# Kernel optimization log

Measured on AMD Instinct MI355X. Metric: run time of the kernel, lower is better.

Reference implementation:

```python
import jax, jax.numpy as jnp
import numpy as np
import math

VOCAB = 390
D = 512
D_INNER = 2048
H = 8
DH = D // H
L = 6
MAX_SEQ = 1024
BATCH = 4
OUT = 2
PAD = 0
EPS = 1e-6


def sinusoid(max_seq, d):
    pos = np.arange(max_seq, dtype=np.float64)[:, None]
    i = np.arange(d, dtype=np.float64)[None, :]
    angle = (pos * np.exp(-np.log(10000.0) * i / d) * np.exp(np.log(10000.0) / d * (i % 2))
             + 0.5 * np.pi * (i % 2))
    return np.sin(angle)[None].astype(np.float32)  # [1, max_seq, d]


def setup_inputs() -> dict:
    key = jax.random.key(0)
    ks = jax.random.split(key, 16)
    s = 0.02
    emb = jax.random.uniform(ks[0], (VOCAB, D), jnp.float32, -0.1, 0.1)
    emb = emb.at[PAD].set(0.0)  # padding_idx row zeroed
    inp = {
        'x': jax.random.randint(ks[1], (BATCH, MAX_SEQ), 0, VOCAB, dtype=jnp.int64) if jax.config.jax_enable_x64 else jax.random.randint(ks[1], (BATCH, MAX_SEQ), 0, VOCAB, dtype=jnp.int32),
        'emb': emb,
        'pos': jnp.asarray(sinusoid(MAX_SEQ, D)),
        'Wq': jax.random.normal(ks[2], (L, D, D), jnp.float32) * s,
        'bq': jnp.zeros((L, D), jnp.float32),
        'Wk': jax.random.normal(ks[3], (L, D, D), jnp.float32) * s,
        'bk': jnp.zeros((L, D), jnp.float32),
        'Wv': jax.random.normal(ks[4], (L, D, D), jnp.float32) * s,
        'bv': jnp.zeros((L, D), jnp.float32),
        'Wo': jax.random.normal(ks[5], (L, D, D), jnp.float32) * s,
        'bo': jnp.zeros((L, D), jnp.float32),
        'E': jax.random.normal(ks[6], (L, MAX_SEQ, DH), jnp.float32),
        'W1': jax.random.normal(ks[7], (L, D, D_INNER), jnp.float32) * s,
        'b1': jnp.zeros((L, D_INNER), jnp.float32),
        'W2': jax.random.normal(ks[8], (L, D_INNER, D), jnp.float32) * s,
        'b2': jnp.zeros((L, D), jnp.float32),
        'ln1_s': jnp.ones((L, D), jnp.float32),
        'ln1_b': jnp.zeros((L, D), jnp.float32),
        'ln2_s': jnp.ones((L, D), jnp.float32),
        'ln2_b': jnp.zeros((L, D), jnp.float32),
        'Wf': jax.random.normal(ks[9], (D, OUT), jnp.float32) * s,
        'bf': jnp.zeros((OUT,), jnp.float32),
    }
    return inp


def _layernorm(x, scale, bias):
    mu = jnp.mean(x, axis=-1, keepdims=True)
    var = jnp.mean(jnp.square(x - mu), axis=-1, keepdims=True)
    return (x - mu) * jax.lax.rsqrt(var + EPS) * scale + bias


def _rel_attention(x, Wq, bq, Wk, bk, Wv, bv, Wo, bo, E):
    b, s, d = x.shape
    q = (x @ Wq + bq).reshape(b, s, H, DH).transpose(0, 2, 1, 3)  # [b,h,s,dh]
    k = (x @ Wk + bk).reshape(b, s, H, DH).transpose(0, 2, 1, 3)
    v = (x @ Wv + bv).reshape(b, s, H, DH).transpose(0, 2, 1, 3)
    m = MAX_SEQ  # len_q == len_k == max_seq -> full E
    QE = jnp.einsum('bhld,md->bhlm', q, E)  # [b,h,s,m]
    # qe masking: keep position j >= m-1-i for query row i
    keep = (jnp.arange(m)[None, :] >= (m - 1 - jnp.arange(s))[:, None]).astype(QE.dtype)
    QE = QE * keep
    # skewing trick: pad-left on last dim, reshape, drop first row
    padded = jnp.pad(QE, ((0, 0), (0, 0), (0, 0), (1, 0)))  # [b,h,s,m+1]
    Srel = padded.reshape(b, H, m + 1, s)[:, :, 1:, :]  # [b,h,m,s] == [b,h,s,s]
    logits = (jnp.einsum('bhqd,bhkd->bhqk', q, k) + Srel) / math.sqrt(DH)
    attn = jax.nn.softmax(logits, axis=-1)
    out = jnp.einsum('bhqk,bhkd->bhqd', attn, v)
    out = out.transpose(0, 2, 1, 3).reshape(b, s, d)
    return out @ Wo + bo


def reference(x, emb, pos, Wq, bq, Wk, bk, Wv, bv, Wo, bo, E, W1, b1, W2, b2,
              ln1_s, ln1_b, ln2_s, ln2_b, Wf, bf):
    h = emb[x] * math.sqrt(D)  # [b,s,d]
    h = h + pos[:, :h.shape[1], :]
    for i in range(L):
        attn = _rel_attention(h, Wq[i], bq[i], Wk[i], bk[i], Wv[i], bv[i], Wo[i], bo[i], E[i])
        h1 = _layernorm(attn + h, ln1_s[i], ln1_b[i])
        ffn = jax.nn.relu(h1 @ W1[i] + b1[i]) @ W2[i] + b2[i]
        h = _layernorm(h1 + ffn, ln2_s[i], ln2_b[i])
    return jnp.tanh(h[:, 0, :] @ Wf + bf)  # [b, OUT]
```

## Files before the change

kernel.cpp:

```cpp
#include <hip/hip_runtime.h>
#include <math.h>

#define BATCH  4
#define SEQ    1024
#define DM     512
#define DI     2048
#define NH     8
#define DH     64
#define NL     6
#define NOUT   2

typedef unsigned short u16;
typedef short s16x8 __attribute__((ext_vector_type(8)));
typedef float f32x4 __attribute__((ext_vector_type(4)));
typedef unsigned short u16x4 __attribute__((ext_vector_type(4)));

#define MFMA16(a, b, c) __builtin_amdgcn_mfma_f32_16x16x32_bf16((a), (b), (c), 0, 0, 0)

static constexpr float SQRT_D = 22.627416997969522f;

#define SLOT_WO   786432
#define SLOT_W1   1048576
#define SLOT_W2   2097152
#define SLOT_E    3145728
#define SLOT_SZ   3211264

__device__ __forceinline__ u16 f2b(float x) {
    union { float f; unsigned u; } v; v.f = x;
    unsigned r = v.u + 0x7fffu + ((v.u >> 16) & 1u);
    return (u16)(r >> 16);
}
__device__ __forceinline__ float b2f(u16 b) {
    union { unsigned u; float f; } v; v.u = ((unsigned)b) << 16; return v.f;
}

__global__ __launch_bounds__(256) void k_embed(const int* __restrict__ x,
                                               const float* __restrict__ emb,
                                               const float* __restrict__ pos,
                                               float* __restrict__ h,
                                               u16* __restrict__ hb) {
    const int idx = blockIdx.x * 256 + threadIdx.x;
    const int d4  = idx & 127;
    const int bs  = idx >> 7;
    const int s   = bs & (SEQ - 1);
    const int tok = x[bs];
    const float4 e = ((const float4*)emb)[tok * 128 + d4];
    const float4 p = ((const float4*)pos)[s * 128 + d4];
    float4 r;
    r.x = e.x * SQRT_D + p.x;  r.y = e.y * SQRT_D + p.y;
    r.z = e.z * SQRT_D + p.z;  r.w = e.w * SQRT_D + p.w;
    ((float4*)h)[idx] = r;
    u16x4 rb = { f2b(r.x), f2b(r.y), f2b(r.z), f2b(r.w) };
    ((u16x4*)hb)[idx] = rb;
}

__global__ __launch_bounds__(256) void k_conv(const float* __restrict__ Wq, const float* __restrict__ Wk,
                                              const float* __restrict__ Wv, const float* __restrict__ Wo,
                                              const float* __restrict__ W1, const float* __restrict__ W2,
                                              const float* __restrict__ E,
                                              u16* __restrict__ wbase, int layer0, int slot_stride) {
    const int ll = blockIdx.x / 3136;
    const int tb = blockIdx.x - ll * 3136;
    const int layer = layer0 + ll;
    u16* Wqkvt = wbase + (size_t)ll * slot_stride;
    u16* Wot   = Wqkvt + SLOT_WO;
    u16* W1t   = Wqkvt + SLOT_W1;
    u16* W2t   = Wqkvt + SLOT_W2;
    u16* Ebf   = Wqkvt + SLOT_E;

    if (tb >= 3072) {
        const int rem = tb - 3072;
        const int idx = rem * 1024 + threadIdx.x * 4;
        const float4 v = *(const float4*)(E + (size_t)layer * SEQ * DH + idx);
        u16x4 o = { f2b(v.x), f2b(v.y), f2b(v.z), f2b(v.w) };
        *(u16x4*)(Ebf + idx) = o;
        return;
    }
    __shared__ float T[32][33];
    const float* src; u16* dst; int Ksz, Nsz, tk, tn;
    if (tb < 768) {
        const int mat = tb >> 8, rem = tb & 255;
        src = (mat == 0 ? Wq : (mat == 1 ? Wk : Wv)) + (size_t)layer * DM * DM;
        dst = Wqkvt + (size_t)mat * DM * DM;
        Ksz = 512; Nsz = 512; tk = rem & 15; tn = rem >> 4;
    } else if (tb < 1024) {
        const int rem = tb - 768;
        src = Wo + (size_t)layer * DM * DM; dst = Wot;
        Ksz = 512; Nsz = 512; tk = rem & 15; tn = rem >> 4;
    } else if (tb < 2048) {
        const int rem = tb - 1024;
        src = W1 + (size_t)layer * DM * DI; dst = W1t;
        Ksz = 512; Nsz = 2048; tk = rem & 15; tn = rem >> 4;
    } else {
        const int rem = tb - 2048;
        src = W2 + (size_t)layer * DI * DM; dst = W2t;
        Ksz = 2048; Nsz = 512; tk = rem >> 4; tn = rem & 15;
    }
    {
        const int rr = threadIdx.x >> 3, c4 = (threadIdx.x & 7) << 2;
        const float4 v = *(const float4*)(src + (size_t)(tk * 32 + rr) * Nsz + tn * 32 + c4);
        T[rr][c4 + 0] = v.x; T[rr][c4 + 1] = v.y; T[rr][c4 + 2] = v.z; T[rr][c4 + 3] = v.w;
    }
    __syncthreads();
    {
        const int nl = threadIdx.x >> 3, k4 = (threadIdx.x & 7) << 2;
        u16x4 o = { f2b(T[k4 + 0][nl]), f2b(T[k4 + 1][nl]), f2b(T[k4 + 2][nl]), f2b(T[k4 + 3][nl]) };
        *(u16x4*)(dst + (size_t)(tn * 32 + nl) * Ksz + tk * 32 + k4) = o;
    }
}

__global__ __launch_bounds__(256) void k_vt(const u16* __restrict__ vb,
                                            u16* __restrict__ Vt) {
    __shared__ float T[32][33];
    const int tn = blockIdx.x;
    const int tk = blockIdx.y;
    const int b  = blockIdx.z;
    const u16* src = vb + (size_t)b * SEQ * DM;
    u16* dst = Vt + (size_t)b * DM * SEQ;
    {
        const int rr = threadIdx.x >> 3, c4 = (threadIdx.x & 7) << 2;
        const u16x4 v = *(const u16x4*)(src + (size_t)(tk * 32 + rr) * DM + tn * 32 + c4);
        T[rr][c4 + 0] = b2f(v.x); T[rr][c4 + 1] = b2f(v.y);
        T[rr][c4 + 2] = b2f(v.z); T[rr][c4 + 3] = b2f(v.w);
    }
    __syncthreads();
    {
        const int nl = threadIdx.x >> 3, k4 = (threadIdx.x & 7) << 2;
        u16x4 o = { f2b(T[k4 + 0][nl]), f2b(T[k4 + 1][nl]),
                    f2b(T[k4 + 2][nl]), f2b(T[k4 + 3][nl]) };
        *(u16x4*)(dst + (size_t)(tn * 32 + nl) * SEQ + tk * 32 + k4) = o;
    }
}

template <int RELU, int WRITE_BF16>
__global__ __launch_bounds__(256) void k_mm(const u16* __restrict__ A,
                                            const u16* __restrict__ Bt,
                                            const float* __restrict__ bias,
                                            float* __restrict__ Cf0,
                                            float* __restrict__ Cf1,
                                            u16* __restrict__ Cb,
                                            int K, int Kslice, int ldc) {
    __shared__ u16 As[128 * 40];
    __shared__ u16 Bs[128 * 40];

    const int n0 = blockIdx.x << 7;
    const int m0 = blockIdx.y << 7;
    const int zz = blockIdx.z;
    const int t  = threadIdx.x;
    const int lane = t & 63, w = t >> 6;
    const int n16 = lane & 15, quad = lane >> 4;
    const int wr = (w & 1) << 6;
    const int wc = (w >> 1) << 6;

    const f32x4 z = {0.f, 0.f, 0.f, 0.f};
    f32x4 acc[4][4];
#pragma unroll
    for (int i = 0; i < 4; ++i)
#pragma unroll
        for (int j = 0; j < 4; ++j) acc[i][j] = z;

    const int sr = t >> 2, sk = (t & 3) << 3;
    const int koff = zz * Kslice;
    const u16* Ag = A  + (size_t)(m0 + sr) * K + koff + sk;
    const u16* Bg = Bt + (size_t)(n0 + sr) * K + koff + sk;

    for (int k0 = 0; k0 < Kslice; k0 += 32) {
        __syncthreads();
        *(uint4*)&As[sr * 40 + sk]        = *(const uint4*)(Ag + k0);
        *(uint4*)&As[(sr + 64) * 40 + sk] = *(const uint4*)(Ag + (size_t)64 * K + k0);
        *(uint4*)&Bs[sr * 40 + sk]        = *(const uint4*)(Bg + k0);
        *(uint4*)&Bs[(sr + 64) * 40 + sk] = *(const uint4*)(Bg + (size_t)64 * K + k0);
        __syncthreads();

        s16x8 af[4], bfr[4];
#pragma unroll
        for (int rb = 0; rb < 4; ++rb)
            af[rb] = *(const s16x8*)&As[(wr + rb * 16 + n16) * 40 + quad * 8];
#pragma unroll
        for (int cb = 0; cb < 4; ++cb)
            bfr[cb] = *(const s16x8*)&Bs[(wc + cb * 16 + n16) * 40 + quad * 8];
#pragma unroll
        for (int rb = 0; rb < 4; ++rb)
#pragma unroll
            for (int cb = 0; cb < 4; ++cb)
                acc[rb][cb] = MFMA16(af[rb], bfr[cb], acc[rb][cb]);
    }

    float* Cf = zz ? Cf1 : Cf0;
#pragma unroll
    for (int cb = 0; cb < 4; ++cb) {
        const int col = n0 + wc + cb * 16 + n16;
        const float bv = (zz == 0) ? bias[col] : 0.f;
#pragma unroll
        for (int rb = 0; rb < 4; ++rb) {
#pragma unroll
            for (int rr = 0; rr < 4; ++rr) {
                const int row = m0 + wr + rb * 16 + quad * 4 + rr;
                float v = acc[rb][cb][rr] + bv;
                if (RELU) v = fmaxf(v, 0.f);
                const size_t idx = (size_t)row * ldc + col;
                if (WRITE_BF16) Cb[idx] = f2b(v);
                else            Cf[idx] = v;
            }
        }
    }
}

__global__ __launch_bounds__(256) void k_mm64(const u16* __restrict__ A,
                                              const u16* __restrict__ Bt,
                                              const float* __restrict__ bias0,
                                              const float* __restrict__ bias1,
                                              const float* __restrict__ bias2,
                                              u16* __restrict__ Cb,
                                              int K, int ldc, int seg_shift, size_t seg_stride) {
    __shared__ u16 As[64 * 72];
    __shared__ u16 Bs[128 * 72];

    const int n0 = blockIdx.x << 7;
    const int m0 = blockIdx.y << 6;
    const int t  = threadIdx.x;
    const int lane = t & 63, w = t >> 6;
    const int n16 = lane & 15, quad = lane >> 4;
    const int wc = w << 5;
    const int r = t >> 3, o = (t & 7) << 3;

    const f32x4 z = {0.f, 0.f, 0.f, 0.f};
    f32x4 acc[4][2];
#pragma unroll
    for (int i = 0; i < 4; ++i) { acc[i][0] = z; acc[i][1] = z; }

    const u16* Ag = A  + (size_t)(m0 + r) * K + o;
    const u16* Bg = Bt + (size_t)(n0 + r) * K + o;

    for (int k0 = 0; k0 < K; k0 += 64) {
        __syncthreads();
        *(uint4*)&As[r * 72 + o]        = *(const uint4*)(Ag + k0);
        *(uint4*)&As[(r + 32) * 72 + o] = *(const uint4*)(Ag + (size_t)32 * K + k0);
        *(uint4*)&Bs[r * 72 + o]        = *(const uint4*)(Bg + k0);
        *(uint4*)&Bs[(r + 32) * 72 + o] = *(const uint4*)(Bg + (size_t)32 * K + k0);
        *(uint4*)&Bs[(r + 64) * 72 + o] = *(const uint4*)(Bg + (size_t)64 * K + k0);
        *(uint4*)&Bs[(r + 96) * 72 + o] = *(const uint4*)(Bg + (size_t)96 * K + k0);
        __syncthreads();

#pragma unroll
        for (int ks = 0; ks < 2; ++ks) {
            s16x8 af[4], bfr[2];
#pragma unroll
            for (int rb = 0; rb < 4; ++rb)
                af[rb] = *(const s16x8*)&As[(rb * 16 + n16) * 72 + ks * 32 + quad * 8];
#pragma unroll
            for (int cb = 0; cb < 2; ++cb)
                bfr[cb] = *(const s16x8*)&Bs[(wc + cb * 16 + n16) * 72 + ks * 32 + quad * 8];
#pragma unroll
            for (int rb = 0; rb < 4; ++rb)
#pragma unroll
                for (int cb = 0; cb < 2; ++cb)
                    acc[rb][cb] = MFMA16(af[rb], bfr[cb], acc[rb][cb]);
        }
    }

    const int sel = n0 >> seg_shift;
    const int colbase = (n0 & ((1 << seg_shift) - 1)) + wc;
    const float* bias = (sel == 0) ? bias0 : (sel == 1 ? bias1 : bias2);
    const size_t cbase = (size_t)sel * seg_stride;
#pragma unroll
    for (int cb = 0; cb < 2; ++cb) {
        const int col = colbase + cb * 16 + n16;
        const float bv = bias[col];
#pragma unroll
        for (int rb = 0; rb < 4; ++rb)
#pragma unroll
            for (int rr = 0; rr < 4; ++rr) {
                const int row = m0 + rb * 16 + quad * 4 + rr;
                Cb[cbase + (size_t)row * ldc + col] = f2b(acc[rb][cb][rr] + bv);
            }
    }
}

__global__ __launch_bounds__(256) void k_attn(const u16* __restrict__ Qg,
                                              const u16* __restrict__ Kg,
                                              const u16* __restrict__ Vt,
                                              const u16* __restrict__ Eg,
                                              u16* __restrict__ Og) {
    __shared__ u16 Ks[64 * 72];
    __shared__ u16 Vts[64 * 72];
    __shared__ u16 Ps[64 * 72];
    __shared__ u16 Es[128 * 72];
    __shared__ u16 arena[128 * 72];

    const int i0 = blockIdx.x << 6;
    const int hd = blockIdx.y;
    const int b  = blockIdx.z;
    const int t  = threadIdx.x;
    const int lane = t & 63;
    const int n16 = lane & 15;
    const int quad = lane >> 4;
    const int rw = (t >> 6) << 4;
    const int ir_base = rw + (quad << 2);
    const int a_last = i0 >> 6;
    const int eb0 = 960 - i0;

    const size_t gb  = (size_t)b * SEQ * DM + hd * DH;
    const size_t vtb = ((size_t)b * DM + hd * DH) * SEQ;

    const int r = t >> 3;
    const int o = (t & 7) << 3;

    const u16* qp = Qg + gb + (size_t)(i0 + rw + n16) * DM + quad * 8;
    const s16x8 qa0 = *(const s16x8*)qp;
    const s16x8 qa1 = *(const s16x8*)(qp + 32);

    uint4 kr0 = *(const uint4*)(Kg + gb + (size_t)r * DM + o);
    uint4 kr1 = *(const uint4*)(Kg + gb + (size_t)(r + 32) * DM + o);
    uint4 vr0 = *(const uint4*)(Vt + vtb + (size_t)r * SEQ + o);
    uint4 vr1 = *(const uint4*)(Vt + vtb + (size_t)(r + 32) * SEQ + o);
    int e0i = eb0 + r;        e0i = e0i > 1023 ? 1023 : e0i;
    int e1i = eb0 + r + 32;   e1i = e1i > 1023 ? 1023 : e1i;
    int e2i = eb0 + r + 64;   e2i = e2i > 1023 ? 1023 : e2i;
    int e3i = eb0 + r + 96;   e3i = e3i > 1023 ? 1023 : e3i;
    uint4 er0 = *(const uint4*)(Eg + (size_t)e0i * DH + o);
    uint4 er1 = *(const uint4*)(Eg + (size_t)e1i * DH + o);
    uint4 er2 = *(const uint4*)(Eg + (size_t)e2i * DH + o);
    uint4 er3 = *(const uint4*)(Eg + (size_t)e3i * DH + o);

    const f32x4 z = {0.f, 0.f, 0.f, 0.f};
    f32x4 Oa[4] = {z, z, z, z};
    float l_run[4] = {0.f, 0.f, 0.f, 0.f};

    for (int ct = 0; ct < 16; ++ct) {
        const int c0 = ct << 6;
        const bool active = (ct <= a_last);

        __syncthreads();
        *(uint4*)&Ks[r * 72 + o]         = kr0;
        *(uint4*)&Ks[(r + 32) * 72 + o]  = kr1;
        *(uint4*)&Vts[r * 72 + o]        = vr0;
        *(uint4*)&Vts[(r + 32) * 72 + o] = vr1;
        if (ct == 0) {
            *(uint4*)&Es[r * 72 + o]        = er0;
            *(uint4*)&Es[(r + 32) * 72 + o] = er1;
            *(uint4*)&Es[(r + 64) * 72 + o] = er2;
            *(uint4*)&Es[(r + 96) * 72 + o] = er3;
        } else if (active) {
            const int nb = ((ct + 1) & 1) << 6;
            *(uint4*)&Es[(nb + r) * 72 + o]      = er0;
            *(uint4*)&Es[(nb + r + 32) * 72 + o] = er1;
        }
        if (ct < 15) {
            const int cn = c0 + 64;
            kr0 = *(const uint4*)(Kg + gb + (size_t)(cn + r) * DM + o);
            kr1 = *(const uint4*)(Kg + gb + (size_t)(cn + r + 32) * DM + o);
            vr0 = *(const uint4*)(Vt + vtb + (size_t)r * SEQ + cn + o);
            vr1 = *(const uint4*)(Vt + vtb + (size_t)(r + 32) * SEQ + cn + o);
            if (ct + 1 <= a_last) {
                const int ebn = eb0 + 64 * (ct + 1) + 64;
                int f0 = ebn + r;      f0 = f0 > 1023 ? 1023 : f0;
                int f1 = ebn + r + 32; f1 = f1 > 1023 ? 1023 : f1;
                er0 = *(const uint4*)(Eg + (size_t)f0 * DH + o);
                er1 = *(const uint4*)(Eg + (size_t)f1 * DH + o);
            }
        }
        __syncthreads();

        f32x4 S[4];
#pragma unroll
        for (int cb = 0; cb < 4; ++cb) {
            const s16x8 k0 = *(const s16x8*)&Ks[(cb * 16 + n16) * 72 + quad * 8];
            const s16x8 k1 = *(const s16x8*)&Ks[(cb * 16 + n16) * 72 + quad * 8 + 32];
            S[cb] = MFMA16(qa0, k0, z);
            S[cb] = MFMA16(qa1, k1, S[cb]);
        }

        if (active) {
            if (ct == 0) {
#pragma unroll
                for (int ub = 0; ub < 8; ++ub) {
                    const s16x8 e0 = *(const s16x8*)&Es[(ub * 16 + n16) * 72 + quad * 8];
                    const s16x8 e1 = *(const s16x8*)&Es[(ub * 16 + n16) * 72 + quad * 8 + 32];
                    f32x4 qe = MFMA16(qa0, e0, z);
                    qe = MFMA16(qa1, e1, qe);
                    u16x4 pk = { f2b(qe[0]), f2b(qe[1]), f2b(qe[2]), f2b(qe[3]) };
                    *(u16x4*)&arena[(ub * 16 + n16) * 72 + ir_base] = pk;
                }
            } else {
                const int pb = ((ct + 1) & 1) << 6;
#pragma unroll
                for (int ub = 0; ub < 4; ++ub) {
                    const s16x8 e0 = *(const s16x8*)&Es[(pb + ub * 16 + n16) * 72 + quad * 8];
                    const s16x8 e1 = *(const s16x8*)&Es[(pb + ub * 16 + n16) * 72 + quad * 8 + 32];
                    f32x4 qe = MFMA16(qa0, e0, z);
                    qe = MFMA16(qa1, e1, qe);
                    u16x4 pk = { f2b(qe[0]), f2b(qe[1]), f2b(qe[2]), f2b(qe[3]) };
                    *(u16x4*)&arena[(pb + ub * 16 + n16) * 72 + ir_base] = pk;
                }
            }
            const int dqc = i0 - c0;
            const int rot = ct << 6;
#pragma unroll
            for (int cb = 0; cb < 4; ++cb)
#pragma unroll
                for (int rr = 0; rr < 4; ++rr) {
                    const int ir = ir_base + rr;
                    const int d = cb * 16 + n16 - ir;
                    const float srel = (d <= dqc)
                        ? b2f(arena[((63 + d + rot) & 127) * 72 + ir]) : 0.f;
                    S[cb][rr] = (S[cb][rr] + srel) * 0.125f;
                }
        } else {
#pragma unroll
            for (int cb = 0; cb < 4; ++cb)
#pragma unroll
                for (int rr = 0; rr < 4; ++rr) S[cb][rr] *= 0.125f;
        }

        float p[4][4];
#pragma unroll
        for (int cb = 0; cb < 4; ++cb)
#pragma unroll
            for (int rr = 0; rr < 4; ++rr) p[cb][rr] = __expf(S[cb][rr]);
#pragma unroll
        for (int rr = 0; rr < 4; ++rr) {
            float rs = p[0][rr] + p[1][rr] + p[2][rr] + p[3][rr];
            rs += __shfl_xor(rs, 1, 64);
            rs += __shfl_xor(rs, 2, 64);
            rs += __shfl_xor(rs, 4, 64);
            rs += __shfl_xor(rs, 8, 64);
            l_run[rr] += rs;
        }

#pragma unroll
        for (int cb = 0; cb < 4; ++cb)
#pragma unroll
            for (int rr = 0; rr < 4; ++rr)
                Ps[(ir_base + rr) * 72 + cb * 16 + n16] = f2b(p[cb][rr]);

        const s16x8 pa0 = *(const s16x8*)&Ps[(rw + n16) * 72 + quad * 8];
        const s16x8 pa1 = *(const s16x8*)&Ps[(rw + n16) * 72 + quad * 8 + 32];
#pragma unroll
        for (int db = 0; db < 4; ++db) {
            const s16x8 v0 = *(const s16x8*)&Vts[(db * 16 + n16) * 72 + quad * 8];
            const s16x8 v1 = *(const s16x8*)&Vts[(db * 16 + n16) * 72 + quad * 8 + 32];
            Oa[db] = MFMA16(pa0, v0, Oa[db]);
            Oa[db] = MFMA16(pa1, v1, Oa[db]);
        }
    }

#pragma unroll
    for (int rr = 0; rr < 4; ++rr) l_run[rr] = 1.f / l_run[rr];
#pragma unroll
    for (int db = 0; db < 4; ++db)
#pragma unroll
        for (int rr = 0; rr < 4; ++rr) {
            const int row = i0 + ir_base + rr;
            Og[gb + (size_t)row * DM + db * 16 + n16] = f2b(Oa[db][rr] * l_run[rr]);
        }
}

__global__ __launch_bounds__(256) void k_ln(const float* __restrict__ A,
                                            const float* __restrict__ R,
                                            const float* __restrict__ sc,
                                            const float* __restrict__ bi,
                                            float* __restrict__ Y,
                                            u16* __restrict__ Yb) {
    const int g = threadIdx.x >> 7;
    const int r = (blockIdx.x << 1) + g;
    const int t = threadIdx.x & 127;
    const int w = threadIdx.x >> 6;
    const float4 a = ((const float4*)(A + (size_t)r * DM))[t];
    const float4 b = ((const float4*)(R + (size_t)r * DM))[t];
    float4 v;
    v.x = a.x + b.x; v.y = a.y + b.y; v.z = a.z + b.z; v.w = a.w + b.w;

    float s = v.x + v.y + v.z + v.w;
#pragma unroll
    for (int o = 32; o > 0; o >>= 1) s += __shfl_down(s, o, 64);
    __shared__ float r1[4], r2[4];
    if ((threadIdx.x & 63) == 0) r1[w] = s;
    __syncthreads();
    const float mean = (r1[g << 1] + r1[(g << 1) + 1]) * (1.f / 512.f);

    float4 d;
    d.x = v.x - mean; d.y = v.y - mean; d.z = v.z - mean; d.w = v.w - mean;
    float q = d.x * d.x + d.y * d.y + d.z * d.z + d.w * d.w;
#pragma unroll
    for (int o = 32; o > 0; o >>= 1) q += __shfl_down(q, o, 64);
    if ((threadIdx.x & 63) == 0) r2[w] = q;
    __syncthreads();
    const float rsq = rsqrtf((r2[g << 1] + r2[(g << 1) + 1]) * (1.f / 512.f) + 1e-6f);

    const float4 s4 = ((const float4*)sc)[t];
    const float4 b4 = ((const float4*)bi)[t];
    float4 y;
    y.x = d.x * rsq * s4.x + b4.x;
    y.y = d.y * rsq * s4.y + b4.y;
    y.z = d.z * rsq * s4.z + b4.z;
    y.w = d.w * rsq * s4.w + b4.w;
    ((float4*)(Y + (size_t)r * DM))[t] = y;
    u16x4 yb = { f2b(y.x), f2b(y.y), f2b(y.z), f2b(y.w) };
    ((u16x4*)(Yb + (size_t)r * DM))[t] = yb;
}

__global__ __launch_bounds__(256) void k_ln3(const float* __restrict__ A0,
                                             const float* __restrict__ A1,
                                             const float* __restrict__ R,
                                             const float* __restrict__ sc,
                                             const float* __restrict__ bi,
                                             float* __restrict__ Y,
                                             u16* __restrict__ Yb) {
    const int g = threadIdx.x >> 7;
    const int r = (blockIdx.x << 1) + g;
    const int t = threadIdx.x & 127;
    const int w = threadIdx.x >> 6;
    const float4 a0 = ((const float4*)(A0 + (size_t)r * DM))[t];
    const float4 a1 = ((const float4*)(A1 + (size_t)r * DM))[t];
    const float4 b  = ((const float4*)(R  + (size_t)r * DM))[t];
    float4 v;
    v.x = a0.x + a1.x + b.x; v.y = a0.y + a1.y + b.y;
    v.z = a0.z + a1.z + b.z; v.w = a0.w + a1.w + b.w;

    float s = v.x + v.y + v.z + v.w;
#pragma unroll
    for (int o = 32; o > 0; o >>= 1) s += __shfl_down(s, o, 64);
    __shared__ float r1[4], r2[4];
    if ((threadIdx.x & 63) == 0) r1[w] = s;
    __syncthreads();
    const float mean = (r1[g << 1] + r1[(g << 1) + 1]) * (1.f / 512.f);

    float4 d;
    d.x = v.x - mean; d.y = v.y - mean; d.z = v.z - mean; d.w = v.w - mean;
    float q = d.x * d.x + d.y * d.y + d.z * d.z + d.w * d.w;
#pragma unroll
    for (int o = 32; o > 0; o >>= 1) q += __shfl_down(q, o, 64);
    if ((threadIdx.x & 63) == 0) r2[w] = q;
    __syncthreads();
    const float rsq = rsqrtf((r2[g << 1] + r2[(g << 1) + 1]) * (1.f / 512.f) + 1e-6f);

    const float4 s4 = ((const float4*)sc)[t];
    const float4 b4 = ((const float4*)bi)[t];
    float4 y;
    y.x = d.x * rsq * s4.x + b4.x;
    y.y = d.y * rsq * s4.y + b4.y;
    y.z = d.z * rsq * s4.z + b4.z;
    y.w = d.w * rsq * s4.w + b4.w;
    ((float4*)(Y + (size_t)r * DM))[t] = y;
    u16x4 yb = { f2b(y.x), f2b(y.y), f2b(y.z), f2b(y.w) };
    ((u16x4*)(Yb + (size_t)r * DM))[t] = yb;
}

__global__ __launch_bounds__(512) void k_head(const float* __restrict__ h,
                                              const float* __restrict__ Wf,
                                              const float* __restrict__ bf,
                                              float* __restrict__ out) {
    const int t = threadIdx.x;
    const int w = t >> 6, lane = t & 63;
    const int b = w >> 1, oo = w & 1;
    float s = 0.f;
    for (int d = lane; d < DM; d += 64)
        s += h[(size_t)b * SEQ * DM + d] * Wf[d * NOUT + oo];
#pragma unroll
    for (int o = 32; o > 0; o >>= 1) s += __shfl_down(s, o, 64);
    if (lane == 0) out[b * NOUT + oo] = tanhf(s + bf[oo]);
}

extern "C" void kernel_launch(void* const* d_in, const int* in_sizes, int n_in,
                              void* d_out, int out_size, void* d_ws, size_t ws_size,
                              hipStream_t stream) {
    const int*   x    = (const int*)d_in[0];
    const float* emb  = (const float*)d_in[1];
    const float* pos  = (const float*)d_in[2];
    const float* Wq   = (const float*)d_in[3];
    const float* bq   = (const float*)d_in[4];
    const float* Wk   = (const float*)d_in[5];
    const float* bk   = (const float*)d_in[6];
    const float* Wv   = (const float*)d_in[7];
    const float* bv   = (const float*)d_in[8];
    const float* Wo   = (const float*)d_in[9];
    const float* bo   = (const float*)d_in[10];
    const float* E    = (const float*)d_in[11];
    const float* W1   = (const float*)d_in[12];
    const float* b1   = (const float*)d_in[13];
    const float* W2   = (const float*)d_in[14];
    const float* b2   = (const float*)d_in[15];
    const float* ln1s = (const float*)d_in[16];
    const float* ln1b = (const float*)d_in[17];
    const float* ln2s = (const float*)d_in[18];
    const float* ln2b = (const float*)d_in[19];
    const float* Wf   = (const float*)d_in[20];
    const float* bfp  = (const float*)d_in[21];
    float* out = (float*)d_out;

    char* W = (char*)d_ws;
    float* h    = (float*)(W);
    float* h1   = (float*)(W + (8u  << 20));
    u16*   hb   = (u16*)  (W + (16u << 20));
    u16*   h1b  = (u16*)  (W + (20u << 20));
    u16*   Vt   = h1b;
    u16*   qb   = (u16*)  (W + (24u << 20));
    u16*   kb   = (u16*)  (W + (28u << 20));
    u16*   vb   = (u16*)  (W + (32u << 20));
    u16*   tb   = (u16*)  (W + (36u << 20));
    u16*   midb = qb;
    float* P1   = (float*)(W + (24u << 20));
    u16*   Wb   = (u16*)  (W + (40u << 20));

    const bool all = ws_size >= (size_t)80478208ull;
    const size_t off_p2 = (40ull << 20) + (size_t)(all ? 6 : 1) * SLOT_SZ * 2;
    const bool splitF2 = ws_size >= off_p2 + (8ull << 20);
    float* P2 = (float*)(W + off_p2);

    const int M = BATCH * SEQ;
    const size_t SEG = (size_t)M * DM;

    k_embed<<<(BATCH * SEQ * DM / 4) / 256, 256, 0, stream>>>(x, emb, pos, h, hb);
    if (all)
        k_conv<<<6 * 3136, 256, 0, stream>>>(Wq, Wk, Wv, Wo, W1, W2, E, Wb, 0, SLOT_SZ);

    for (int l = 0; l < NL; ++l) {
        if (!all)
            k_conv<<<3136, 256, 0, stream>>>(Wq, Wk, Wv, Wo, W1, W2, E, Wb, l, 0);
        u16* wl   = Wb + (size_t)(all ? l : 0) * SLOT_SZ;
        u16* wqkv = wl;
        u16* wot  = wl + SLOT_WO;
        u16* w1t  = wl + SLOT_W1;
        u16* w2t  = wl + SLOT_W2;
        u16* ebf  = wl + SLOT_E;

        k_mm64<<<dim3(12, 64), 256, 0, stream>>>(hb, wqkv,
            bq + l * DM, bk + l * DM, bv + l * DM, qb, 512, 512, 9, SEG);
        k_vt<<<dim3(16, 32, 4), 256, 0, stream>>>(vb, Vt);
        k_attn<<<dim3(16, 8, 4), 256, 0, stream>>>(qb, kb, Vt, ebf, tb);
        k_mm<0, 0><<<dim3(4, 32, 2), 256, 0, stream>>>(tb, wot,
            bo + l * DM, h1, P1, nullptr, 512, 256, 512);
        k_ln3<<<M / 2, 256, 0, stream>>>(h1, P1, h, ln1s + l * DM, ln1b + l * DM, h1, h1b);
        k_mm<1, 1><<<dim3(16, 32, 1), 256, 0, stream>>>(h1b, w1t,
            b1 + l * DI, nullptr, nullptr, midb, 512, 512, 2048);
        if (splitF2) {
            k_mm<0, 0><<<dim3(4, 32, 2), 256, 0, stream>>>(midb, w2t,
                b2 + l * DM, h, P2, nullptr, 2048, 1024, 512);
            k_ln3<<<M / 2, 256, 0, stream>>>(h, P2, h1, ln2s + l * DM, ln2b + l * DM, h, hb);
        } else {
            k_mm<0, 0><<<dim3(4, 32, 1), 256, 0, stream>>>(midb, w2t,
                b2 + l * DM, h, nullptr, nullptr, 2048, 2048, 512);
            k_ln<<<M / 2, 256, 0, stream>>>(h, h1, ln2s + l * DM, ln2b + l * DM, h, hb);
        }
    }

    k_head<<<1, 512, 0, stream>>>(h, Wf, bfp, out);
}
```

Before: 1.004 ms.

## Use direct global-to-LDS loads in GEMMs and read E from global in attention

Both GEMM kernels now stage A and B tiles with global_load_lds (16-byte direct loads into LDS), dropping the padded LDS stride to an unpadded 32-element stride. k_mm64 also shrinks its K step from 64 to 32. In the attention kernel, the E staging buffer and its register prefetch are removed, and MFMA operands for the relative-position term are loaded directly from global memory. This is meant to cut register traffic and LDS footprint, but risks LDS bank conflicts from the unpadded layout, more barriers per K, and longer-latency unprefetched global reads of E.

```diff
diff --git a/kernel.cpp b/kernel.cpp
--- a/kernel.cpp
+++ b/kernel.cpp
@@ -32,6 +32,12 @@
 }
 __device__ __forceinline__ float b2f(u16 b) {
     union { unsigned u; float f; } v; v.u = ((unsigned)b) << 16; return v.f;
+}
+
+__device__ __forceinline__ void gll16(const u16* g, const u16* l) {
+    __builtin_amdgcn_global_load_lds(
+        (const __attribute__((address_space(1))) unsigned int*)g,
+        (__attribute__((address_space(3))) unsigned int*)l, 16, 0, 0);
 }
 
 __global__ __launch_bounds__(256) void k_embed(const int* __restrict__ x,
@@ -140,8 +146,8 @@
                                             float* __restrict__ Cf1,
                                             u16* __restrict__ Cb,
                                             int K, int Kslice, int ldc) {
-    __shared__ u16 As[128 * 40];
-    __shared__ u16 Bs[128 * 40];
+    __shared__ u16 As[128 * 32];
+    __shared__ u16 Bs[128 * 32];
 
     const int n0 = blockIdx.x << 7;
     const int m0 = blockIdx.y << 7;
@@ -151,6 +157,7 @@
     const int n16 = lane & 15, quad = lane >> 4;
     const int wr = (w & 1) << 6;
     const int wc = (w >> 1) << 6;
+    const int w16 = w << 4;
 
     const f32x4 z = {0.f, 0.f, 0.f, 0.f};
     f32x4 acc[4][4];
@@ -163,22 +170,24 @@
     const int koff = zz * Kslice;
     const u16* Ag = A  + (size_t)(m0 + sr) * K + koff + sk;
     const u16* Bg = Bt + (size_t)(n0 + sr) * K + koff + sk;
+    u16* Asw = As + w16 * 32;
+    u16* Bsw = Bs + w16 * 32;
 
     for (int k0 = 0; k0 < Kslice; k0 += 32) {
         __syncthreads();
-        *(uint4*)&As[sr * 40 + sk]        = *(const uint4*)(Ag + k0);
-        *(uint4*)&As[(sr + 64) * 40 + sk] = *(const uint4*)(Ag + (size_t)64 * K + k0);
-        *(uint4*)&Bs[sr * 40 + sk]        = *(const uint4*)(Bg + k0);
-        *(uint4*)&Bs[(sr + 64) * 40 + sk] = *(const uint4*)(Bg + (size_t)64 * K + k0);
+        gll16(Ag + k0,                    Asw);
+        gll16(Ag + (size_t)64 * K + k0,   Asw + 64 * 32);
+        gll16(Bg + k0,                    Bsw);
+        gll16(Bg + (size_t)64 * K + k0,   Bsw + 64 * 32);
         __syncthreads();
 
         s16x8 af[4], bfr[4];
 #pragma unroll
         for (int rb = 0; rb < 4; ++rb)
-            af[rb] = *(const s16x8*)&As[(wr + rb * 16 + n16) * 40 + quad * 8];
+            af[rb] = *(const s16x8*)&As[(wr + rb * 16 + n16) * 32 + quad * 8];
 #pragma unroll
         for (int cb = 0; cb < 4; ++cb)
-            bfr[cb] = *(const s16x8*)&Bs[(wc + cb * 16 + n16) * 40 + quad * 8];
+            bfr[cb] = *(const s16x8*)&Bs[(wc + cb * 16 + n16) * 32 + quad * 8];
 #pragma unroll
         for (int rb = 0; rb < 4; ++rb)
 #pragma unroll
@@ -213,8 +222,8 @@
                                               const float* __restrict__ bias2,
                                               u16* __restrict__ Cb,
                                               int K, int ldc, int seg_shift, size_t seg_stride) {
-    __shared__ u16 As[64 * 72];
-    __shared__ u16 Bs[128 * 72];
+    __shared__ u16 As[64 * 32];
+    __shared__ u16 Bs[128 * 32];
 
     const int n0 = blockIdx.x << 7;
     const int m0 = blockIdx.y << 6;
@@ -222,41 +231,38 @@
     const int lane = t & 63, w = t >> 6;
     const int n16 = lane & 15, quad = lane >> 4;
     const int wc = w << 5;
-    const int r = t >> 3, o = (t & 7) << 3;
+    const int w16 = w << 4;
 
     const f32x4 z = {0.f, 0.f, 0.f, 0.f};
     f32x4 acc[4][2];
 #pragma unroll
     for (int i = 0; i < 4; ++i) { acc[i][0] = z; acc[i][1] = z; }
 
-    const u16* Ag = A  + (size_t)(m0 + r) * K + o;
-    const u16* Bg = Bt + (size_t)(n0 + r) * K + o;
-
-    for (int k0 = 0; k0 < K; k0 += 64) {
+    const int sr = t >> 2, sk = (t & 3) << 3;
+    const u16* Ag = A  + (size_t)(m0 + sr) * K + sk;
+    const u16* Bg = Bt + (size_t)(n0 + sr) * K + sk;
+    u16* Asw = As + w16 * 32;
+    u16* Bsw = Bs + w16 * 32;
+
+    for (int k0 = 0; k0 < K; k0 += 32) {
         __syncthreads();
-        *(uint4*)&As[r * 72 + o]        = *(const uint4*)(Ag + k0);
-        *(uint4*)&As[(r + 32) * 72 + o] = *(const uint4*)(Ag + (size_t)32 * K + k0);
-        *(uint4*)&Bs[r * 72 + o]        = *(const uint4*)(Bg + k0);
-        *(uint4*)&Bs[(r + 32) * 72 + o] = *(const uint4*)(Bg + (size_t)32 * K + k0);
-        *(uint4*)&Bs[(r + 64) * 72 + o] = *(const uint4*)(Bg + (size_t)64 * K + k0);
-        *(uint4*)&Bs[(r + 96) * 72 + o] = *(const uint4*)(Bg + (size_t)96 * K + k0);
+        gll16(Ag + k0,                  Asw);
+        gll16(Bg + k0,                  Bsw);
+        gll16(Bg + (size_t)64 * K + k0, Bsw + 64 * 32);
         __syncthreads();
 
-#pragma unroll
-        for (int ks = 0; ks < 2; ++ks) {
-            s16x8 af[4], bfr[2];
-#pragma unroll
-            for (int rb = 0; rb < 4; ++rb)
-                af[rb] = *(const s16x8*)&As[(rb * 16 + n16) * 72 + ks * 32 + quad * 8];
+        s16x8 af[4], bfr[2];
+#pragma unroll
+        for (int rb = 0; rb < 4; ++rb)
+            af[rb] = *(const s16x8*)&As[(rb * 16 + n16) * 32 + quad * 8];
+#pragma unroll
+        for (int cb = 0; cb < 2; ++cb)
+            bfr[cb] = *(const s16x8*)&Bs[(wc + cb * 16 + n16) * 32 + quad * 8];
+#pragma unroll
+        for (int rb = 0; rb < 4; ++rb)
 #pragma unroll
             for (int cb = 0; cb < 2; ++cb)
-                bfr[cb] = *(const s16x8*)&Bs[(wc + cb * 16 + n16) * 72 + ks * 32 + quad * 8];
-#pragma unroll
-            for (int rb = 0; rb < 4; ++rb)
-#pragma unroll
-                for (int cb = 0; cb < 2; ++cb)
-                    acc[rb][cb] = MFMA16(af[rb], bfr[cb], acc[rb][cb]);
-        }
+                acc[rb][cb] = MFMA16(af[rb], bfr[cb], acc[rb][cb]);
     }
 
     const int sel = n0 >> seg_shift;
@@ -285,7 +291,6 @@
     __shared__ u16 Ks[64 * 72];
     __shared__ u16 Vts[64 * 72];
     __shared__ u16 Ps[64 * 72];
-    __shared__ u16 Es[128 * 72];
     __shared__ u16 arena[128 * 72];
 
     const int i0 = blockIdx.x << 6;
@@ -314,14 +319,6 @@
     uint4 kr1 = *(const uint4*)(Kg + gb + (size_t)(r + 32) * DM + o);
     uint4 vr0 = *(const uint4*)(Vt + vtb + (size_t)r * SEQ + o);
     uint4 vr1 = *(const uint4*)(Vt + vtb + (size_t)(r + 32) * SEQ + o);
-    int e0i = eb0 + r;        e0i = e0i > 1023 ? 1023 : e0i;
-    int e1i = eb0 + r + 32;   e1i = e1i > 1023 ? 1023 : e1i;
-    int e2i = eb0 + r + 64;   e2i = e2i > 1023 ? 1023 : e2i;
-    int e3i = eb0 + r + 96;   e3i = e3i > 1023 ? 1023 : e3i;
-    uint4 er0 = *(const uint4*)(Eg + (size_t)e0i * DH + o);
-    uint4 er1 = *(const uint4*)(Eg + (size_t)e1i * DH + o);
-    uint4 er2 = *(const uint4*)(Eg + (size_t)e2i * DH + o);
-    uint4 er3 = *(const uint4*)(Eg + (size_t)e3i * DH + o);
 
     const f32x4 z = {0.f, 0.f, 0.f, 0.f};
     f32x4 Oa[4] = {z, z, z, z};
@@ -336,29 +333,12 @@
         *(uint4*)&Ks[(r + 32) * 72 + o]  = kr1;
         *(uint4*)&Vts[r * 72 + o]        = vr0;
         *(uint4*)&Vts[(r + 32) * 72 + o] = vr1;
-        if (ct == 0) {
-            *(uint4*)&Es[r * 72 + o]        = er0;
-            *(uint4*)&Es[(r + 32) * 72 + o] = er1;
-            *(uint4*)&Es[(r + 64) * 72 + o] = er2;
-            *(uint4*)&Es[(r + 96) * 72 + o] = er3;
-        } else if (active) {
-            const int nb = ((ct + 1) & 1) << 6;
-            *(uint4*)&Es[(nb + r) * 72 + o]      = er0;
-            *(uint4*)&Es[(nb + r + 32) * 72 + o] = er1;
-        }
         if (ct < 15) {
             const int cn = c0 + 64;
             kr0 = *(const uint4*)(Kg + gb + (size_t)(cn + r) * DM + o);
             kr1 = *(const uint4*)(Kg + gb + (size_t)(cn + r + 32) * DM + o);
             vr0 = *(const uint4*)(Vt + vtb + (size_t)r * SEQ + cn + o);
             vr1 = *(const uint4*)(Vt + vtb + (size_t)(r + 32) * SEQ + cn + o);
-            if (ct + 1 <= a_last) {
-                const int ebn = eb0 + 64 * (ct + 1) + 64;
-                int f0 = ebn + r;      f0 = f0 > 1023 ? 1023 : f0;
-                int f1 = ebn + r + 32; f1 = f1 > 1023 ? 1023 : f1;
-                er0 = *(const uint4*)(Eg + (size_t)f0 * DH + o);
-                er1 = *(const uint4*)(Eg + (size_t)f1 * DH + o);
-            }
         }
         __syncthreads();
 
@@ -372,13 +352,14 @@
         }
 
         if (active) {
+            const int eb = eb0 + c0;
             if (ct == 0) {
 #pragma unroll
                 for (int ub = 0; ub < 8; ++ub) {
-                    const s16x8 e0 = *(const s16x8*)&Es[(ub * 16 + n16) * 72 + quad * 8];
-                    const s16x8 e1 = *(const s16x8*)&Es[(ub * 16 + n16) * 72 + quad * 8 + 32];
-                    f32x4 qe = MFMA16(qa0, e0, z);
-                    qe = MFMA16(qa1, e1, qe);
+                    int er = eb + ub * 16 + n16; er = er > 1023 ? 1023 : er;
+                    const u16* ep = Eg + (size_t)er * DH + quad * 8;
+                    f32x4 qe = MFMA16(qa0, *(const s16x8*)ep, z);
+                    qe = MFMA16(qa1, *(const s16x8*)(ep + 32), qe);
                     u16x4 pk = { f2b(qe[0]), f2b(qe[1]), f2b(qe[2]), f2b(qe[3]) };
                     *(u16x4*)&arena[(ub * 16 + n16) * 72 + ir_base] = pk;
                 }
@@ -386,10 +367,10 @@
                 const int pb = ((ct + 1) & 1) << 6;
 #pragma unroll
                 for (int ub = 0; ub < 4; ++ub) {
-                    const s16x8 e0 = *(const s16x8*)&Es[(pb + ub * 16 + n16) * 72 + quad * 8];
-                    const s16x8 e1 = *(const s16x8*)&Es[(pb + ub * 16 + n16) * 72 + quad * 8 + 32];
-                    f32x4 qe = MFMA16(qa0, e0, z);
-                    qe = MFMA16(qa1, e1, qe);
+                    int er = eb + 64 + ub * 16 + n16; er = er > 1023 ? 1023 : er;
+                    const u16* ep = Eg + (size_t)er * DH + quad * 8;
+                    f32x4 qe = MFMA16(qa0, *(const s16x8*)ep, z);
+                    qe = MFMA16(qa1, *(const s16x8*)(ep + 32), qe);
                     u16x4 pk = { f2b(qe[0]), f2b(qe[1]), f2b(qe[2]), f2b(qe[3]) };
                     *(u16x4*)&arena[(pb + ub * 16 + n16) * 72 + ir_base] = pk;
                 }
```

New measurement: 1.105 ms. +10.1%, slower.
